# Performance work log

Measured on AMD Instinct MI355X. Metric: run time of the kernel, lower is better.

Reference implementation:

```python
import jax, jax.numpy as jnp
import numpy as np

B, S, D = 16, 2048, 1024   # batch, src_len, per-tensor feature dim (input_dim*growth_factor)
OUT = 1024                 # output_dim


def setup_inputs() -> dict:
    key = jax.random.key(0)
    k1, k2, k3, k4, k5, k6 = jax.random.split(key, 6)
    hidden = jax.random.normal(k1, (B, S, D), dtype=jnp.float32)
    encoder_outputs = jax.random.normal(k2, (B, S, D), dtype=jnp.float32)
    c_t = jax.random.normal(k3, (B, D), dtype=jnp.float32)
    # Linear(input_dim*3*growth_factor=3*D, OUT): PyTorch stores weight as [OUT, 3D]
    limit = 1.0 / np.sqrt(3 * D)
    W = jax.random.uniform(k4, (OUT, 3 * D), minval=-limit, maxval=limit, dtype=jnp.float32)
    b = jax.random.uniform(k5, (OUT,), minval=-limit, maxval=limit, dtype=jnp.float32)
    v = jax.random.uniform(k6, (OUT,), dtype=jnp.float32)  # torch.rand -> U[0,1)
    return {"hidden": hidden, "encoder_outputs": encoder_outputs, "c_t": c_t,
            "W": W, "b": b, "v": v}


def reference(hidden, encoder_outputs, c_t, W, b, v):
    # c_t broadcast over src_len; concat on feature dim -> [B, S, 3D]
    c_rep = jnp.broadcast_to(c_t[:, None, :], hidden.shape)
    cat = jnp.concatenate((hidden, c_rep, encoder_outputs), axis=2)
    # energy = relu(cat @ W^T + b): [B, S, OUT]
    energy = jax.nn.relu(jnp.einsum('bsf,of->bso', cat, W) + b)
    # attention = energy @ v: [B, S], then softmax over src_len
    attention = jnp.einsum('bso,o->bs', energy, v)
    return jax.nn.softmax(attention, axis=1)
```

## Files before the change

kernel.cpp:

```cpp
#include <hip/hip_runtime.h>
#include <hip/hip_bf16.h>


typedef __attribute__((ext_vector_type(8))) short short8;
typedef __attribute__((ext_vector_type(4))) float f32x4;
typedef __attribute__((ext_vector_type(8))) unsigned short ushort8v;
typedef __attribute__((ext_vector_type(4))) unsigned short ushort4v;

#define NB 16
#define NS 2048
#define ND 1024
#define NOUT 1024
#define NM (NB * NS)
#define KHE 2048
#define TM 128
#define TN 128
#define BK 64

#define PREP_ACONV 16384
#define PREP_WCONV 2048
#define PREP_CBIAS 256
#define PREP_ZERO 32

__device__ __forceinline__ unsigned short bf16_rne(float x) {
    unsigned int u = __float_as_uint(x);
    unsigned int r = (u + 0x7fffu + ((u >> 16) & 1u)) >> 16;
    return (unsigned short)r;
}

__device__ __forceinline__ void gload_lds16(const unsigned short* g, unsigned short* l) {
    __builtin_amdgcn_global_load_lds(
        (const __attribute__((address_space(1))) void*)g,
        (__attribute__((address_space(3))) void*)l, 16, 0, 0);
}

__global__ __launch_bounds__(256) void prep_k(const float* __restrict__ hidden,
                                              const float* __restrict__ enc,
                                              const float* __restrict__ c_t,
                                              const float* __restrict__ W,
                                              const float* __restrict__ bias,
                                              unsigned short* __restrict__ Abf,
                                              unsigned short* __restrict__ Wbf,
                                              float* __restrict__ cbias,
                                              float* __restrict__ logits) {
    const int bid = blockIdx.x;
    const int tid = threadIdx.x;
    if (bid < PREP_ACONV) {
        size_t c = (size_t)bid * 256 + tid;
        size_t m = c >> 7;
        int k = (int)(c & 127) * 16;
        const float* src = (k < ND) ? (hidden + m * ND + k) : (enc + m * ND + (k - ND));
        float4 f0 = ((const float4*)src)[0];
        float4 f1 = ((const float4*)src)[1];
        float4 f2 = ((const float4*)src)[2];
        float4 f3 = ((const float4*)src)[3];
        ushort8v h0, h1;
        h0[0] = bf16_rne(f0.x); h0[1] = bf16_rne(f0.y); h0[2] = bf16_rne(f0.z); h0[3] = bf16_rne(f0.w);
        h0[4] = bf16_rne(f1.x); h0[5] = bf16_rne(f1.y); h0[6] = bf16_rne(f1.z); h0[7] = bf16_rne(f1.w);
        h1[0] = bf16_rne(f2.x); h1[1] = bf16_rne(f2.y); h1[2] = bf16_rne(f2.z); h1[3] = bf16_rne(f2.w);
        h1[4] = bf16_rne(f3.x); h1[5] = bf16_rne(f3.y); h1[6] = bf16_rne(f3.z); h1[7] = bf16_rne(f3.w);
        *(ushort8v*)(Abf + m * KHE + k) = h0;
        *(ushort8v*)(Abf + m * KHE + k + 8) = h1;
    } else if (bid < PREP_ACONV + PREP_WCONV) {
        int idx = (bid - PREP_ACONV) * 256 + tid;
        int o = idx >> 9;
        int k = (idx & 511) * 4;
        int off = (k < ND) ? k : (k + ND);
        float4 f = *(const float4*)(W + (size_t)o * 3072 + off);
        ushort4v h;
        h.x = bf16_rne(f.x); h.y = bf16_rne(f.y); h.z = bf16_rne(f.z); h.w = bf16_rne(f.w);
        *(ushort4v*)(Wbf + (size_t)o * KHE + k) = h;
    } else if (bid < PREP_ACONV + PREP_WCONV + PREP_CBIAS) {
        int o = (bid - PREP_ACONV - PREP_WCONV) * 4 + (tid >> 6);
        int lane = tid & 63;
        const float* w = W + (size_t)o * 3072 + ND;
        float wr[16];
        #pragma unroll
        for (int j = 0; j < 16; ++j) wr[j] = w[lane + j * 64];
        float bo = bias[o];
        for (int b = 0; b < NB; ++b) {
            const float* cc = c_t + (size_t)b * ND;
            float s = 0.f;
            #pragma unroll
            for (int j = 0; j < 16; ++j) s = fmaf(cc[lane + j * 64], wr[j], s);
            #pragma unroll
            for (int m = 1; m < 64; m <<= 1) s += __shfl_xor(s, m);
            if (lane == 0) cbias[b * NOUT + o] = s + bo;
        }
    } else {
        int idx = (bid - PREP_ACONV - PREP_WCONV - PREP_CBIAS) * 256 + tid;
        ((float4*)logits)[idx] = make_float4(0.f, 0.f, 0.f, 0.f);
    }
}

__global__ __launch_bounds__(256) void wconv_k(const float* __restrict__ W,
                                               unsigned short* __restrict__ Wbf) {
    int idx = blockIdx.x * 256 + threadIdx.x;
    int o = idx >> 9;
    int k = (idx & 511) * 4;
    int off = (k < ND) ? k : (k + ND);
    float4 f = *(const float4*)(W + (size_t)o * 3072 + off);
    ushort4v h;
    h.x = bf16_rne(f.x); h.y = bf16_rne(f.y); h.z = bf16_rne(f.z); h.w = bf16_rne(f.w);
    *(ushort4v*)(Wbf + (size_t)o * KHE + k) = h;
}

__global__ __launch_bounds__(256) void cbias_k(const float* __restrict__ c_t,
                                               const float* __restrict__ W,
                                               const float* __restrict__ bias,
                                               float* __restrict__ cbias) {
    int o = blockIdx.x * 4 + (threadIdx.x >> 6);
    int lane = threadIdx.x & 63;
    const float* w = W + (size_t)o * 3072 + ND;
    float wr[16];
    #pragma unroll
    for (int j = 0; j < 16; ++j) wr[j] = w[lane + j * 64];
    float bo = bias[o];
    for (int b = 0; b < NB; ++b) {
        const float* c = c_t + (size_t)b * ND;
        float s = 0.f;
        #pragma unroll
        for (int j = 0; j < 16; ++j) s = fmaf(c[lane + j * 64], wr[j], s);
        #pragma unroll
        for (int m = 1; m < 64; m <<= 1) s += __shfl_xor(s, m);
        if (lane == 0) cbias[b * NOUT + o] = s + bo;
    }
}

__global__ __launch_bounds__(256) void gemm_att_bf_k(const unsigned short* __restrict__ Abf,
                                                     const unsigned short* __restrict__ Wbf,
                                                     const float* __restrict__ cbias,
                                                     const float* __restrict__ v,
                                                     float* __restrict__ logits) {
    __shared__ unsigned short As[TM * BK] __attribute__((aligned(16)));
    __shared__ unsigned short Bs[TN * BK] __attribute__((aligned(16)));
    __shared__ float rowsum[2][TM];
    __shared__ float cb_s[TN];
    __shared__ float v_s[TN];

    const int tid = threadIdx.x;
    const int ntile = blockIdx.x & 7;
    const int mtile = blockIdx.x >> 3;
    const int m0 = mtile * TM;
    const int o0 = ntile * TN;
    const int batch = m0 >> 11;

    if (tid < TN) {
        cb_s[tid] = cbias[batch * NOUT + o0 + tid];
        v_s[tid] = v[o0 + tid];
    }

    const int wid = tid >> 6;
    const int lane = tid & 63;
    const int wm = (wid & 1) * 64;
    const int wn = (wid >> 1) * 64;

    const int srow = lane >> 3;
    const int schunk = (lane & 7) ^ srow;
    const unsigned short* agb = Abf + (size_t)(m0 + wid * 32 + srow) * KHE + schunk * 8;
    const unsigned short* bgb = Wbf + (size_t)(o0 + wid * 32 + srow) * KHE + schunk * 8;
    unsigned short* alb = As + (wid * 32) * BK;
    unsigned short* blb = Bs + (wid * 32) * BK;

    f32x4 acc[4][4] = {};

    for (int kt = 0; kt < KHE; kt += BK) {
        #pragma unroll
        for (int t = 0; t < 4; ++t) {
            gload_lds16(agb + (size_t)(t * 8) * KHE + kt, alb + (t * 8) * BK);
            gload_lds16(bgb + (size_t)(t * 8) * KHE + kt, blb + (t * 8) * BK);
        }
        __syncthreads();

        #pragma unroll
        for (int s = 0; s < 2; ++s) {
            const int cbase = s * 4 + (lane >> 4);
            short8 a_frag[4], b_frag[4];
            #pragma unroll
            for (int i = 0; i < 4; ++i) {
                int row = wm + i * 16 + (lane & 15);
                a_frag[i] = *(const short8*)(As + row * BK + ((cbase ^ (row & 7)) * 8));
            }
            #pragma unroll
            for (int j = 0; j < 4; ++j) {
                int row = wn + j * 16 + (lane & 15);
                b_frag[j] = *(const short8*)(Bs + row * BK + ((cbase ^ (row & 7)) * 8));
            }
            #pragma unroll
            for (int i = 0; i < 4; ++i)
                #pragma unroll
                for (int j = 0; j < 4; ++j)
                    acc[i][j] = __builtin_amdgcn_mfma_f32_16x16x32_bf16(a_frag[i], b_frag[j],
                                                                        acc[i][j], 0, 0, 0);
        }
        __syncthreads();
    }

    const int col = lane & 15;
    const int q = lane >> 4;
    float vv[4], cbv[4];
    #pragma unroll
    for (int j = 0; j < 4; ++j) {
        int oc = wn + j * 16 + col;
        vv[j] = v_s[oc];
        cbv[j] = cb_s[oc];
    }
    #pragma unroll
    for (int i = 0; i < 4; ++i) {
        #pragma unroll
        for (int r = 0; r < 4; ++r) {
            float s = 0.f;
            #pragma unroll
            for (int j = 0; j < 4; ++j) {
                float e = acc[i][j][r] + cbv[j];
                e = fmaxf(e, 0.f);
                s = fmaf(e, vv[j], s);
            }
            s += __shfl_xor(s, 1);
            s += __shfl_xor(s, 2);
            s += __shfl_xor(s, 4);
            s += __shfl_xor(s, 8);
            if (col == 0) rowsum[wid >> 1][wm + i * 16 + q * 4 + r] = s;
        }
    }
    __syncthreads();
    if (tid < TM) atomicAdd(&logits[m0 + tid], rowsum[0][tid] + rowsum[1][tid]);
}

__global__ __launch_bounds__(256) void gemm_att_k(const float* __restrict__ hidden,
                                                  const float* __restrict__ enc,
                                                  const unsigned short* __restrict__ Wbf,
                                                  const float* __restrict__ Wf,
                                                  const float* __restrict__ cbias,
                                                  const float* __restrict__ v,
                                                  float* __restrict__ logits,
                                                  int use_wbf) {
    __shared__ unsigned short As[TM * 32] __attribute__((aligned(16)));
    __shared__ unsigned short Bs[TN * 32] __attribute__((aligned(16)));
    __shared__ float rowsum[2][TM];
    __shared__ float cb_s[TN];
    __shared__ float v_s[TN];

    const int tid = threadIdx.x;
    const int ntile = blockIdx.x & 7;
    const int mtile = blockIdx.x >> 3;
    const int m0 = mtile * TM;
    const int o0 = ntile * TN;
    const int batch = m0 >> 11;

    if (tid < TN) {
        cb_s[tid] = cbias[batch * NOUT + o0 + tid];
        v_s[tid] = v[o0 + tid];
    }

    const int wid = tid >> 6;
    const int lane = tid & 63;
    const int wm = (wid & 1) * 64;
    const int wn = (wid >> 1) * 64;

    f32x4 acc[4][4] = {};

    for (int kt = 0; kt < KHE; kt += 32) {
        const float* Abase = (kt < ND) ? hidden : enc;
        const int aoff = (kt < ND) ? kt : (kt - ND);
        #pragma unroll
        for (int i = 0; i < 4; ++i) {
            int p = tid + i * 256;
            int row = p >> 3, kc = p & 7;
            float4 f = *(const float4*)(Abase + (size_t)(m0 + row) * ND + aoff + kc * 4);
            ushort4v h;
            h.x = bf16_rne(f.x); h.y = bf16_rne(f.y); h.z = bf16_rne(f.z); h.w = bf16_rne(f.w);
            *(ushort4v*)(As + row * 32 + kc * 4) = h;
        }
        if (use_wbf) {
            #pragma unroll
            for (int i = 0; i < 2; ++i) {
                int u = tid + i * 256;
                int ol = u >> 2, kc = u & 3;
                ushort8v w8 = *(const ushort8v*)(Wbf + (size_t)(o0 + ol) * KHE + kt + kc * 8);
                *(ushort8v*)(Bs + ol * 32 + kc * 8) = w8;
            }
        } else {
            const int woff = (kt < ND) ? kt : (kt + ND);
            #pragma unroll
            for (int i = 0; i < 4; ++i) {
                int p = tid + i * 256;
                int row = p >> 3, kc = p & 7;
                float4 f = *(const float4*)(Wf + (size_t)(o0 + row) * 3072 + woff + kc * 4);
                ushort4v h;
                h.x = bf16_rne(f.x); h.y = bf16_rne(f.y); h.z = bf16_rne(f.z); h.w = bf16_rne(f.w);
                *(ushort4v*)(Bs + row * 32 + kc * 4) = h;
            }
        }
        __syncthreads();

        short8 a_frag[4], b_frag[4];
        #pragma unroll
        for (int i = 0; i < 4; ++i)
            a_frag[i] = *(const short8*)(As + (wm + i * 16 + (lane & 15)) * 32 + (lane >> 4) * 8);
        #pragma unroll
        for (int j = 0; j < 4; ++j)
            b_frag[j] = *(const short8*)(Bs + (wn + j * 16 + (lane & 15)) * 32 + (lane >> 4) * 8);
        #pragma unroll
        for (int i = 0; i < 4; ++i)
            #pragma unroll
            for (int j = 0; j < 4; ++j)
                acc[i][j] = __builtin_amdgcn_mfma_f32_16x16x32_bf16(a_frag[i], b_frag[j],
                                                                    acc[i][j], 0, 0, 0);
        __syncthreads();
    }

    const int col = lane & 15;
    const int q = lane >> 4;
    float vv[4], cbv[4];
    #pragma unroll
    for (int j = 0; j < 4; ++j) {
        int oc = wn + j * 16 + col;
        vv[j] = v_s[oc];
        cbv[j] = cb_s[oc];
    }
    #pragma unroll
    for (int i = 0; i < 4; ++i) {
        #pragma unroll
        for (int r = 0; r < 4; ++r) {
            float s = 0.f;
            #pragma unroll
            for (int j = 0; j < 4; ++j) {
                float e = acc[i][j][r] + cbv[j];
                e = fmaxf(e, 0.f);
                s = fmaf(e, vv[j], s);
            }
            s += __shfl_xor(s, 1);
            s += __shfl_xor(s, 2);
            s += __shfl_xor(s, 4);
            s += __shfl_xor(s, 8);
            if (col == 0) rowsum[wid >> 1][wm + i * 16 + q * 4 + r] = s;
        }
    }
    __syncthreads();
    if (tid < TM) atomicAdd(&logits[m0 + tid], rowsum[0][tid] + rowsum[1][tid]);
}

__global__ __launch_bounds__(256) void softmax_k(const float* __restrict__ logits,
                                                 float* __restrict__ out) {
    const int b = blockIdx.x;
    const int tid = threadIdx.x;
    const int lane = tid & 63, wid = tid >> 6;
    __shared__ float redmax[4];
    __shared__ float redsum[4];
    const float* L = logits + (size_t)b * NS;
    float x[8];
    float mx = -3.4e38f;
    #pragma unroll
    for (int i = 0; i < 8; ++i) {
        x[i] = L[tid + i * 256];
        mx = fmaxf(mx, x[i]);
    }
    #pragma unroll
    for (int m = 1; m < 64; m <<= 1) mx = fmaxf(mx, __shfl_xor(mx, m));
    if (lane == 0) redmax[wid] = mx;
    __syncthreads();
    mx = fmaxf(fmaxf(redmax[0], redmax[1]), fmaxf(redmax[2], redmax[3]));
    float sum = 0.f;
    #pragma unroll
    for (int i = 0; i < 8; ++i) {
        x[i] = expf(x[i] - mx);
        sum += x[i];
    }
    #pragma unroll
    for (int m = 1; m < 64; m <<= 1) sum += __shfl_xor(sum, m);
    if (lane == 0) redsum[wid] = sum;
    __syncthreads();
    float inv = 1.0f / (redsum[0] + redsum[1] + redsum[2] + redsum[3]);
    #pragma unroll
    for (int i = 0; i < 8; ++i) out[(size_t)b * NS + tid + i * 256] = x[i] * inv;
}

extern "C" void kernel_launch(void* const* d_in, const int* in_sizes, int n_in,
                              void* d_out, int out_size, void* d_ws, size_t ws_size,
                              hipStream_t stream) {
    const float* hidden = (const float*)d_in[0];
    const float* enc    = (const float*)d_in[1];
    const float* c_t    = (const float*)d_in[2];
    const float* W      = (const float*)d_in[3];
    const float* bias   = (const float*)d_in[4];
    const float* v      = (const float*)d_in[5];
    float* out = (float*)d_out;

    char* ws = (char*)d_ws;
    float* logits = (float*)ws;
    float* cbias  = (float*)(ws + 131072);
    unsigned short* Wbf = (unsigned short*)(ws + 196608);
    unsigned short* Abf = (unsigned short*)(ws + 196608 + 4194304);
    const size_t need_wbf = 196608 + (size_t)NOUT * KHE * 2;
    const size_t need_abf = need_wbf + (size_t)NM * KHE * 2;

    if (ws_size >= need_abf) {
        prep_k<<<PREP_ACONV + PREP_WCONV + PREP_CBIAS + PREP_ZERO, 256, 0, stream>>>(
            hidden, enc, c_t, W, bias, Abf, Wbf, cbias, logits);
        gemm_att_bf_k<<<(NM / TM) * (NOUT / TN), 256, 0, stream>>>(Abf, Wbf, cbias, v, logits);
    } else if (ws_size >= need_wbf) {
        hipMemsetAsync(logits, 0, NM * sizeof(float), stream);
        cbias_k<<<NOUT / 4, 256, 0, stream>>>(c_t, W, bias, cbias);
        wconv_k<<<(NOUT * KHE / 4) / 256, 256, 0, stream>>>(W, Wbf);
        gemm_att_k<<<(NM / TM) * (NOUT / TN), 256, 0, stream>>>(hidden, enc, Wbf, W, cbias, v,
                                                                logits, 1);
    } else {
        hipMemsetAsync(logits, 0, NM * sizeof(float), stream);
        cbias_k<<<NOUT / 4, 256, 0, stream>>>(c_t, W, bias, cbias);
        gemm_att_k<<<(NM / TM) * (NOUT / TN), 256, 0, stream>>>(hidden, enc, Wbf, W, cbias, v,
                                                                logits, 0);
    }
    softmax_k<<<NB, 256, 0, stream>>>(logits, out);
}
```

Measured before the change: 481.7 us.

## Double-buffer LDS K-slabs and remap blocks for XCD-local M tiles

The GEMM main loop now splits K into 32-wide slabs held in two LDS buffers. The global-to-LDS load of the next slab is issued before computing on the current one, which overlaps memory latency with MFMA work and removes one barrier per iteration. Block IDs are also remapped so each XCD handles a contiguous range of M tiles across all 8 N tiles, improving L2 reuse of A rows. Trade-offs: smaller slabs mean more loop iterations and barriers per K, and the new swizzle must stay correct for the 32-wide layout.

```diff
diff --git a/kernel.cpp b/kernel.cpp
--- a/kernel.cpp
+++ b/kernel.cpp
@@ -15,7 +15,8 @@
 #define KHE 2048
 #define TM 128
 #define TN 128
-#define BK 64
+#define BKP 32
+#define NSLAB (KHE / BKP)
 
 #define PREP_ACONV 16384
 #define PREP_WCONV 2048
@@ -132,15 +133,18 @@
                                                      const float* __restrict__ cbias,
                                                      const float* __restrict__ v,
                                                      float* __restrict__ logits) {
-    __shared__ unsigned short As[TM * BK] __attribute__((aligned(16)));
-    __shared__ unsigned short Bs[TN * BK] __attribute__((aligned(16)));
+    __shared__ unsigned short As[2][TM * BKP] __attribute__((aligned(16)));
+    __shared__ unsigned short Bs[2][TN * BKP] __attribute__((aligned(16)));
     __shared__ float rowsum[2][TM];
     __shared__ float cb_s[TN];
     __shared__ float v_s[TN];
 
     const int tid = threadIdx.x;
-    const int ntile = blockIdx.x & 7;
-    const int mtile = blockIdx.x >> 3;
+    const int bid = blockIdx.x;
+    const int xcd = bid & 7;
+    const int slot = bid >> 3;
+    const int mtile = xcd * 32 + (slot >> 3);
+    const int ntile = slot & 7;
     const int m0 = mtile * TM;
     const int o0 = ntile * TN;
     const int batch = m0 >> 11;
@@ -155,45 +159,49 @@
     const int wm = (wid & 1) * 64;
     const int wn = (wid >> 1) * 64;
 
-    const int srow = lane >> 3;
-    const int schunk = (lane & 7) ^ srow;
-    const unsigned short* agb = Abf + (size_t)(m0 + wid * 32 + srow) * KHE + schunk * 8;
-    const unsigned short* bgb = Wbf + (size_t)(o0 + wid * 32 + srow) * KHE + schunk * 8;
-    unsigned short* alb = As + (wid * 32) * BK;
-    unsigned short* blb = Bs + (wid * 32) * BK;
+    const int srow = lane >> 2;
+    const int schunk = (lane & 3) ^ (srow & 3);
+    const unsigned short* agA0 = Abf + (size_t)(m0 + wid * 16 + srow) * KHE + schunk * 8;
+    const unsigned short* agA1 = agA0 + (size_t)64 * KHE;
+    const unsigned short* bgB0 = Wbf + (size_t)(o0 + wid * 16 + srow) * KHE + schunk * 8;
+    const unsigned short* bgB1 = bgB0 + (size_t)64 * KHE;
+    const int ldsA0 = (wid * 16) * BKP;
+    const int ldsA1 = (64 + wid * 16) * BKP;
 
     f32x4 acc[4][4] = {};
 
-    for (int kt = 0; kt < KHE; kt += BK) {
-        #pragma unroll
-        for (int t = 0; t < 4; ++t) {
-            gload_lds16(agb + (size_t)(t * 8) * KHE + kt, alb + (t * 8) * BK);
-            gload_lds16(bgb + (size_t)(t * 8) * KHE + kt, blb + (t * 8) * BK);
-        }
+    gload_lds16(agA0, &As[0][ldsA0]);
+    gload_lds16(agA1, &As[0][ldsA1]);
+    gload_lds16(bgB0, &Bs[0][ldsA0]);
+    gload_lds16(bgB1, &Bs[0][ldsA1]);
+
+    for (int s = 0; s < NSLAB; ++s) {
         __syncthreads();
-
-        #pragma unroll
-        for (int s = 0; s < 2; ++s) {
-            const int cbase = s * 4 + (lane >> 4);
-            short8 a_frag[4], b_frag[4];
-            #pragma unroll
-            for (int i = 0; i < 4; ++i) {
-                int row = wm + i * 16 + (lane & 15);
-                a_frag[i] = *(const short8*)(As + row * BK + ((cbase ^ (row & 7)) * 8));
-            }
-            #pragma unroll
-            for (int j = 0; j < 4; ++j) {
-                int row = wn + j * 16 + (lane & 15);
-                b_frag[j] = *(const short8*)(Bs + row * BK + ((cbase ^ (row & 7)) * 8));
-            }
-            #pragma unroll
-            for (int i = 0; i < 4; ++i)
-                #pragma unroll
-                for (int j = 0; j < 4; ++j)
-                    acc[i][j] = __builtin_amdgcn_mfma_f32_16x16x32_bf16(a_frag[i], b_frag[j],
-                                                                        acc[i][j], 0, 0, 0);
-        }
-        __syncthreads();
+        if (s < NSLAB - 1) {
+            const int ktn = (s + 1) * BKP;
+            unsigned short* An = As[(s + 1) & 1];
+            unsigned short* Bn = Bs[(s + 1) & 1];
+            gload_lds16(agA0 + ktn, An + ldsA0);
+            gload_lds16(agA1 + ktn, An + ldsA1);
+            gload_lds16(bgB0 + ktn, Bn + ldsA0);
+            gload_lds16(bgB1 + ktn, Bn + ldsA1);
+        }
+        const unsigned short* Ac = As[s & 1];
+        const unsigned short* Bc = Bs[s & 1];
+        const int fslot = ((lane >> 4) ^ (lane & 3)) * 8;
+        short8 a_frag[4], b_frag[4];
+        #pragma unroll
+        for (int i = 0; i < 4; ++i)
+            a_frag[i] = *(const short8*)(Ac + (wm + i * 16 + (lane & 15)) * BKP + fslot);
+        #pragma unroll
+        for (int j = 0; j < 4; ++j)
+            b_frag[j] = *(const short8*)(Bc + (wn + j * 16 + (lane & 15)) * BKP + fslot);
+        #pragma unroll
+        for (int i = 0; i < 4; ++i)
+            #pragma unroll
+            for (int j = 0; j < 4; ++j)
+                acc[i][j] = __builtin_amdgcn_mfma_f32_16x16x32_bf16(a_frag[i], b_frag[j],
+                                                                    acc[i][j], 0, 0, 0);
     }
 
     const int col = lane & 15;
```

Result: slower. 504.3 us (+4.7%).
